# Kernel optimization log

Measured on AMD Instinct MI355X. Metric: run time of the kernel, lower is better.

The kernel has to match this reference:

```python
import jax, jax.numpy as jnp
import numpy as np

LEVELS = [(100, 128), (50, 64), (25, 32), (13, 16), (7, 8)]
B, C, S = 16, 80, 17064  # batch, class_num, sum(h*w)
GAMMA, ALPHA = 2.0, 0.25


def setup_inputs() -> dict:
    key = jax.random.key(0)
    ks = iter(jax.random.split(key, 40))
    inp = {}
    for i, (h, w) in enumerate(LEVELS):
        inp[f"cls_p{i}"] = jax.random.normal(next(ks), (B, C, h, w), dtype=jnp.float32)
        inp[f"cnt_p{i}"] = jax.random.normal(next(ks), (B, 1, h, w), dtype=jnp.float32)
        inp[f"reg_p{i}"] = jax.random.uniform(next(ks), (B, 4, h, w), dtype=jnp.float32) * 8.0 + 0.1
    keep = jax.random.uniform(next(ks), (B, S, 1)) > 0.7
    cnt_val = jax.random.uniform(next(ks), (B, S, 1), dtype=jnp.float32)
    inp["cnt_targets"] = jnp.where(keep, cnt_val, -1.0)
    inp["reg_targets"] = jax.random.uniform(next(ks), (B, S, 4), dtype=jnp.float32) * 8.0 + 0.1
    inp["cls_targets"] = jax.random.randint(next(ks), (B, S, 1), 0, 81, dtype=jnp.int64)
    return inp


def _flatten_levels(preds, c):
    # each pred [B,c,h,w] -> [B,h*w,c]; concat over levels -> [B,S,c]
    return jnp.concatenate(
        [p.transpose(0, 2, 3, 1).reshape(p.shape[0], -1, c) for p in preds], axis=1)


def _fcos_loss(cls_ps, cnt_ps, reg_ps, cls_t, cnt_t, reg_t):
    mask = (cnt_t > -1.0)[..., 0]                       # [B,S] bool positive mask
    num_pos = jnp.clip(jnp.sum(mask, axis=1), 1).astype(jnp.float32)  # [B]

    # ---- focal cls loss (over ALL locations, as in the original) ----
    cls = _flatten_levels(cls_ps, C)                    # [B,S,C]
    onehot = (jnp.arange(1, C + 1)[None, None, :] == cls_t).astype(jnp.float32)
    p = jax.nn.sigmoid(cls)
    p_t = onehot * p + (1.0 - onehot) * (1.0 - p)
    alpha_f = onehot * ALPHA + (1.0 - onehot) * (1.0 - ALPHA)
    focal = -alpha_f * (1.0 - p_t) ** GAMMA * jnp.log(p_t)
    cls_loss = jnp.mean(jnp.sum(focal, axis=(1, 2)) / num_pos)

    # ---- centerness BCE-with-logits, masked sum ----
    cnt = _flatten_levels(cnt_ps, 1)[..., 0]            # [B,S]
    t = cnt_t[..., 0]
    bce = jnp.maximum(cnt, 0.0) - cnt * t + jnp.log1p(jnp.exp(-jnp.abs(cnt)))
    cnt_loss = jnp.mean(jnp.sum(bce * mask, axis=1) / num_pos)

    # ---- GIoU reg loss, masked sum ----
    reg = _flatten_levels(reg_ps, 4)                    # [B,S,4] ltrb offsets
    lt_min = jnp.minimum(reg[..., :2], reg_t[..., :2])
    rb_min = jnp.minimum(reg[..., 2:], reg_t[..., 2:])
    wh_min = jnp.clip(rb_min + lt_min, 0.0)
    overlap = wh_min[..., 0] * wh_min[..., 1]
    area1 = (reg[..., 2] + reg[..., 0]) * (reg[..., 3] + reg[..., 1])
    area2 = (reg_t[..., 2] + reg_t[..., 0]) * (reg_t[..., 3] + reg_t[..., 1])
    union = area1 + area2 - overlap
    iou = overlap / union
    lt_max = jnp.maximum(reg[..., :2], reg_t[..., :2])
    rb_max = jnp.maximum(reg[..., 2:], reg_t[..., 2:])
    wh_max = jnp.clip(rb_max + lt_max, 0.0)
    g_area = wh_max[..., 0] * wh_max[..., 1]
    giou = iou - (g_area - union) / jnp.clip(g_area, 1e-10)
    reg_loss = jnp.mean(jnp.sum((1.0 - giou) * mask, axis=1) / num_pos)

    total = cls_loss + cnt_loss + reg_loss  # add_centerness=True
    return (cls_loss, cnt_loss, reg_loss, total)


def reference(cls_p0, cls_p1, cls_p2, cls_p3, cls_p4,
              cnt_p0, cnt_p1, cnt_p2, cnt_p3, cnt_p4,
              reg_p0, reg_p1, reg_p2, reg_p3, reg_p4,
              cnt_targets, reg_targets, cls_targets):
    return _fcos_loss([cls_p0, cls_p1, cls_p2, cls_p3, cls_p4],
                      [cnt_p0, cnt_p1, cnt_p2, cnt_p3, cnt_p4],
                      [reg_p0, reg_p1, reg_p2, reg_p3, reg_p4],
                      cls_targets, cnt_targets, reg_targets)
```

## Files before the change

### kernel.cpp

```cpp
#include <hip/hip_runtime.h>

#define S_TOTAL 17064
#define NB 16
#define NC 80
#define QPB 4266
#define NXQ 17
#define NCCH 20
#define NCH (NCCH + 1)
#define TOTAL_BLOCKS (NXQ * NCH * NB)
#define P1 TOTAL_BLOCKS
#define P2 (2 * TOTAL_BLOCKS)

typedef float vfloat4 __attribute__((ext_vector_type(4)));

struct Ptrs {
    const float* cls[5];
    const float* cnt[5];
    const float* reg[5];
    const float* cnt_t;
    const float* reg_t;
    const int*   cls_t;
    float*       ws;
    float*       out;
};

__device__ __forceinline__ float focal_term(float x, bool o) {
    const float xs = o ? x : -x;
    const float af = o ? 0.25f : 0.75f;
    const float em = __expf(-xs);
    const float pt = 1.0f / (1.0f + em);
    const float q  = em * pt;
    return af * q * q * __logf(1.0f + em);
}

__device__ __forceinline__ float giou_term(float pl, float pt_, float pr, float pb,
                                           float tl, float tt, float tr, float tb) {
    const float overlap = fmaxf(fminf(pr, tr) + fminf(pl, tl), 0.0f) *
                          fmaxf(fminf(pb, tb) + fminf(pt_, tt), 0.0f);
    const float area1 = (pr + pl) * (pb + pt_);
    const float area2 = (tr + tl) * (tb + tt);
    const float uni = area1 + area2 - overlap;
    const float iou = overlap / uni;
    const float ga = fmaxf(fmaxf(pr, tr) + fmaxf(pl, tl), 0.0f) *
                     fmaxf(fmaxf(pb, tb) + fmaxf(pt_, tt), 0.0f);
    const float giou = iou - (ga - uni) / fmaxf(ga, 1e-10f);
    return 1.0f - giou;
}

__device__ __forceinline__ float bce_term(float x, float t) {
    return fmaxf(x, 0.0f) - x * t + __logf(1.0f + __expf(-fabsf(x)));
}

__global__ __launch_bounds__(256) void fcos_main(Ptrs p) {
    const int xq = blockIdx.x;
    const int ch = blockIdx.y;
    const int b  = blockIdx.z;
    const int fq = xq * 256 + (int)threadIdx.x;

    int lvl, qb, hw, off;
    if (fq < 3200)      { lvl = 0; qb = 0;    hw = 12800; off = 0;     }
    else if (fq < 4000) { lvl = 1; qb = 3200; hw = 3200;  off = 12800; }
    else if (fq < 4200) { lvl = 2; qb = 4000; hw = 800;   off = 16000; }
    else if (fq < 4252) { lvl = 3; qb = 4200; hw = 208;   off = 16800; }
    else                { lvl = 4; qb = 4252; hw = 56;    off = 17008; }
    const bool active = (fq < QPB);

    float r0 = 0.f, r1 = 0.f, r2 = 0.f;

    if (active) {
        const int s0  = (fq - qb) << 2;
        const int gs0 = b * S_TOTAL + off + s0;

        if (ch < NCCH) {
            const int c0 = ch * 4;
            const int4 tq = *(const int4*)(p.cls_t + gs0);
            const float* cp = p.cls[lvl] + (size_t)((b * NC + c0) * hw + s0);

            vfloat4 buf[4];
            #pragma unroll
            for (int j = 0; j < 4; ++j)
                buf[j] = *(const vfloat4*)(cp + (size_t)(j * hw));

            float a0 = 0.f, a1 = 0.f, a2 = 0.f, a3 = 0.f;
            #pragma unroll
            for (int j = 0; j < 4; ++j) {
                const int c1 = c0 + j + 1;
                a0 += focal_term(buf[j].x, tq.x == c1);
                a1 += focal_term(buf[j].y, tq.y == c1);
                a2 += focal_term(buf[j].z, tq.z == c1);
                a3 += focal_term(buf[j].w, tq.w == c1);
            }
            r0 = (a0 + a1) + (a2 + a3);
        } else {
            const float4 tC  = *(const float4*)(p.cnt_t + gs0);
            const float4 xc  = *(const float4*)(p.cnt[lvl] + (size_t)(b * hw + s0));
            const float m0 = (tC.x > -1.0f) ? 1.0f : 0.0f;
            const float m1 = (tC.y > -1.0f) ? 1.0f : 0.0f;
            const float m2 = (tC.z > -1.0f) ? 1.0f : 0.0f;
            const float m3 = (tC.w > -1.0f) ? 1.0f : 0.0f;
            r2 = m0 + m1 + m2 + m3;
            r0 = bce_term(xc.x, tC.x) * m0 + bce_term(xc.y, tC.y) * m1 +
                 bce_term(xc.z, tC.z) * m2 + bce_term(xc.w, tC.w) * m3;

            const float* rp  = p.reg[lvl] + (size_t)(b * 4 * hw + s0);
            const float4 pl  = *(const float4*)(rp);
            const float4 pt_ = *(const float4*)(rp + (size_t)hw);
            const float4 pr  = *(const float4*)(rp + (size_t)(2 * hw));
            const float4 pb  = *(const float4*)(rp + (size_t)(3 * hw));
            const float4 t0  = *(const float4*)(p.reg_t + (size_t)(gs0 + 0) * 4);
            const float4 t1  = *(const float4*)(p.reg_t + (size_t)(gs0 + 1) * 4);
            const float4 t2  = *(const float4*)(p.reg_t + (size_t)(gs0 + 2) * 4);
            const float4 t3  = *(const float4*)(p.reg_t + (size_t)(gs0 + 3) * 4);

            r1 = giou_term(pl.x, pt_.x, pr.x, pb.x, t0.x, t0.y, t0.z, t0.w) * m0 +
                 giou_term(pl.y, pt_.y, pr.y, pb.y, t1.x, t1.y, t1.z, t1.w) * m1 +
                 giou_term(pl.z, pt_.z, pr.z, pb.z, t2.x, t2.y, t2.z, t2.w) * m2 +
                 giou_term(pl.w, pt_.w, pr.w, pb.w, t3.x, t3.y, t3.z, t3.w) * m3;
        }
    }

    #pragma unroll
    for (int d = 32; d; d >>= 1) {
        r0 += __shfl_down(r0, d);
        r1 += __shfl_down(r1, d);
        r2 += __shfl_down(r2, d);
    }

    __shared__ float red[3][4];
    const int wave = threadIdx.x >> 6;
    const int lane = threadIdx.x & 63;
    if (lane == 0) {
        red[0][wave] = r0;
        red[1][wave] = r1;
        red[2][wave] = r2;
    }
    __syncthreads();
    if (threadIdx.x == 0) {
        const int bid = xq + NXQ * (ch + NCH * b);
        p.ws[bid]      = red[0][0] + red[0][1] + red[0][2] + red[0][3];
        p.ws[P1 + bid] = red[1][0] + red[1][1] + red[1][2] + red[1][3];
        p.ws[P2 + bid] = red[2][0] + red[2][1] + red[2][2] + red[2][3];
    }
}

__global__ __launch_bounds__(512) void fcos_finalize(const float* __restrict__ ws,
                                                     float* __restrict__ out) {
    __shared__ float sA[NB * NCH];
    __shared__ float sB[NB * NCH];
    __shared__ float sC[NB * NCH];
    __shared__ float lb[3][NB];
    const int t = (int)threadIdx.x;

    if (t < NB * NCH) {
        const int b = t / NCH, ch = t - b * NCH;
        const int base = NXQ * (ch + NCH * b);
        float q0 = 0.f, q1 = 0.f, q2 = 0.f;
        #pragma unroll
        for (int xq = 0; xq < NXQ; ++xq) {
            q0 += ws[base + xq];
            q1 += ws[P1 + base + xq];
            q2 += ws[P2 + base + xq];
        }
        sA[t] = q0; sB[t] = q1; sC[t] = q2;
    }
    __syncthreads();

    if (t < NB) {
        const int rowbase = t * NCH;
        float cls = 0.f, reg = 0.f, pos = 0.f;
        #pragma unroll
        for (int ch = 0; ch < NCCH; ++ch) cls += sA[rowbase + ch];
        const float cnt = sA[rowbase + NCCH];
        #pragma unroll
        for (int ch = 0; ch < NCH; ++ch) { reg += sB[rowbase + ch]; pos += sC[rowbase + ch]; }
        const float np = fmaxf(pos, 1.0f);
        lb[0][t] = cls / np;
        lb[1][t] = cnt / np;
        lb[2][t] = reg / np;
    }
    __syncthreads();

    if (t == 0) {
        float l0 = 0.f, l1 = 0.f, l2 = 0.f;
        #pragma unroll
        for (int b = 0; b < NB; ++b) {
            l0 += lb[0][b]; l1 += lb[1][b]; l2 += lb[2][b];
        }
        l0 *= (1.0f / NB); l1 *= (1.0f / NB); l2 *= (1.0f / NB);
        out[0] = l0;
        out[1] = l1;
        out[2] = l2;
        out[3] = l0 + l1 + l2;
    }
}

extern "C" void kernel_launch(void* const* d_in, const int* in_sizes, int n_in,
                              void* d_out, int out_size, void* d_ws, size_t ws_size,
                              hipStream_t stream) {
    Ptrs p;
    for (int i = 0; i < 5; ++i) {
        p.cls[i] = (const float*)d_in[3 * i + 0];
        p.cnt[i] = (const float*)d_in[3 * i + 1];
        p.reg[i] = (const float*)d_in[3 * i + 2];
    }
    p.cnt_t = (const float*)d_in[15];
    p.reg_t = (const float*)d_in[16];
    p.cls_t = (const int*)  d_in[17];
    p.ws    = (float*)d_ws;
    p.out   = (float*)d_out;

    dim3 grid(NXQ, NCH, NB);
    fcos_main<<<grid, 256, 0, stream>>>(p);
    fcos_finalize<<<dim3(1), 512, 0, stream>>>((const float*)d_ws, (float*)d_out);
}
```

Measured before the change: 152.7 us.

## Regroup work into 7 channel chunks per block, folding cnt/reg into last chunk

Each block now processes 12 classification channels (8 in the last chunk) and the last chunk also computes the centerness and GIoU terms, in place of 20 four-channel class blocks plus a separate cnt/reg block. This cuts the grid from 21 to 7 chunks per position tile and reloads class targets less often, with more work per thread. The finalize kernel changes to a strided 256-thread reduction over four partial arrays. The risks are fewer blocks to hide latency with, and imbalance because the last chunk carries the extra cnt/reg work.

After: 149.1 us. 1.02x faster.

```diff
diff --git a/kernel.cpp b/kernel.cpp
--- a/kernel.cpp
+++ b/kernel.cpp
@@ -5,11 +5,9 @@
 #define NC 80
 #define QPB 4266
 #define NXQ 17
-#define NCCH 20
-#define NCH (NCCH + 1)
-#define TOTAL_BLOCKS (NXQ * NCH * NB)
-#define P1 TOTAL_BLOCKS
-#define P2 (2 * TOTAL_BLOCKS)
+#define NJ 7
+#define TOTAL_BLOCKS (NB * NJ * NXQ)
+#define PL TOTAL_BLOCKS
 
 typedef float vfloat4 __attribute__((ext_vector_type(4)));
 
@@ -52,10 +50,12 @@
 }
 
 __global__ __launch_bounds__(256) void fcos_main(Ptrs p) {
-    const int xq = blockIdx.x;
-    const int ch = blockIdx.y;
-    const int b  = blockIdx.z;
-    const int fq = xq * 256 + (int)threadIdx.x;
+    const int bid = (int)blockIdx.x;
+    const int b   = bid / (NJ * NXQ);
+    const int r   = bid - b * (NJ * NXQ);
+    const int j   = r / NXQ;
+    const int xq  = r - j * NXQ;
+    const int fq  = xq * 256 + (int)threadIdx.x;
 
     int lvl, qb, hw, off;
     if (fq < 3200)      { lvl = 0; qb = 0;    hw = 12800; off = 0;     }
@@ -65,42 +65,39 @@
     else                { lvl = 4; qb = 4252; hw = 56;    off = 17008; }
     const bool active = (fq < QPB);
 
-    float r0 = 0.f, r1 = 0.f, r2 = 0.f;
+    float acls = 0.f, acnt = 0.f, areg = 0.f, apos = 0.f;
 
     if (active) {
         const int s0  = (fq - qb) << 2;
         const int gs0 = b * S_TOTAL + off + s0;
-
-        if (ch < NCCH) {
-            const int c0 = ch * 4;
-            const int4 tq = *(const int4*)(p.cls_t + gs0);
-            const float* cp = p.cls[lvl] + (size_t)((b * NC + c0) * hw + s0);
-
-            vfloat4 buf[4];
-            #pragma unroll
-            for (int j = 0; j < 4; ++j)
-                buf[j] = *(const vfloat4*)(cp + (size_t)(j * hw));
-
-            float a0 = 0.f, a1 = 0.f, a2 = 0.f, a3 = 0.f;
-            #pragma unroll
-            for (int j = 0; j < 4; ++j) {
-                const int c1 = c0 + j + 1;
-                a0 += focal_term(buf[j].x, tq.x == c1);
-                a1 += focal_term(buf[j].y, tq.y == c1);
-                a2 += focal_term(buf[j].z, tq.z == c1);
-                a3 += focal_term(buf[j].w, tq.w == c1);
-            }
-            r0 = (a0 + a1) + (a2 + a3);
-        } else {
+        const int4 tq = *(const int4*)(p.cls_t + gs0);
+
+        const int cbase = j * 12;
+        const int ncls  = (j < 6) ? 12 : 8;
+        const float* cp = p.cls[lvl] + (size_t)((b * NC + cbase) * hw + s0);
+
+        float a0 = 0.f, a1 = 0.f, a2 = 0.f, a3 = 0.f;
+        #pragma unroll 4
+        for (int c = 0; c < ncls; ++c) {
+            const vfloat4 v = *(const vfloat4*)(cp + (size_t)(c * hw));
+            const int c1 = cbase + c + 1;
+            a0 += focal_term(v.x, tq.x == c1);
+            a1 += focal_term(v.y, tq.y == c1);
+            a2 += focal_term(v.z, tq.z == c1);
+            a3 += focal_term(v.w, tq.w == c1);
+        }
+        acls = (a0 + a1) + (a2 + a3);
+
+        if (j == 6) {
             const float4 tC  = *(const float4*)(p.cnt_t + gs0);
             const float4 xc  = *(const float4*)(p.cnt[lvl] + (size_t)(b * hw + s0));
             const float m0 = (tC.x > -1.0f) ? 1.0f : 0.0f;
             const float m1 = (tC.y > -1.0f) ? 1.0f : 0.0f;
             const float m2 = (tC.z > -1.0f) ? 1.0f : 0.0f;
             const float m3 = (tC.w > -1.0f) ? 1.0f : 0.0f;
-            r2 = m0 + m1 + m2 + m3;
-            r0 = bce_term(xc.x, tC.x) * m0 + bce_term(xc.y, tC.y) * m1 +
-                 bce_term(xc.z, tC.z) * m2 + bce_term(xc.w, tC.w) * m3;
+            apos = m0 + m1 + m2 + m3;
+            acnt = bce_term(xc.x, tC.x) * m0 + bce_term(xc.y, tC.y) * m1 +
+                   bce_term(xc.z, tC.z) * m2 + bce_term(xc.w, tC.w) * m3;
 
             const float* rp  = p.reg[lvl] + (size_t)(b * 4 * hw + s0);
             const float4 pl  = *(const float4*)(rp);
@@ -112,67 +109,67 @@
             const float4 t2  = *(const float4*)(p.reg_t + (size_t)(gs0 + 2) * 4);
             const float4 t3  = *(const float4*)(p.reg_t + (size_t)(gs0 + 3) * 4);
 
-            r1 = giou_term(pl.x, pt_.x, pr.x, pb.x, t0.x, t0.y, t0.z, t0.w) * m0 +
-                 giou_term(pl.y, pt_.y, pr.y, pb.y, t1.x, t1.y, t1.z, t1.w) * m1 +
-                 giou_term(pl.z, pt_.z, pr.z, pb.z, t2.x, t2.y, t2.z, t2.w) * m2 +
-                 giou_term(pl.w, pt_.w, pr.w, pb.w, t3.x, t3.y, t3.z, t3.w) * m3;
+            areg = giou_term(pl.x, pt_.x, pr.x, pb.x, t0.x, t0.y, t0.z, t0.w) * m0 +
+                   giou_term(pl.y, pt_.y, pr.y, pb.y, t1.x, t1.y, t1.z, t1.w) * m1 +
+                   giou_term(pl.z, pt_.z, pr.z, pb.z, t2.x, t2.y, t2.z, t2.w) * m2 +
+                   giou_term(pl.w, pt_.w, pr.w, pb.w, t3.x, t3.y, t3.z, t3.w) * m3;
         }
     }
 
     #pragma unroll
     for (int d = 32; d; d >>= 1) {
-        r0 += __shfl_down(r0, d);
-        r1 += __shfl_down(r1, d);
-        r2 += __shfl_down(r2, d);
-    }
-
-    __shared__ float red[3][4];
+        acls += __shfl_down(acls, d);
+        acnt += __shfl_down(acnt, d);
+        areg += __shfl_down(areg, d);
+        apos += __shfl_down(apos, d);
+    }
+
+    __shared__ float red[4][4];
     const int wave = threadIdx.x >> 6;
     const int lane = threadIdx.x & 63;
     if (lane == 0) {
-        red[0][wave] = r0;
-        red[1][wave] = r1;
-        red[2][wave] = r2;
+        red[0][wave] = acls;
+        red[1][wave] = acnt;
+        red[2][wave] = areg;
+        red[3][wave] = apos;
     }
     __syncthreads();
     if (threadIdx.x == 0) {
-        const int bid = xq + NXQ * (ch + NCH * b);
-        p.ws[bid]      = red[0][0] + red[0][1] + red[0][2] + red[0][3];
-        p.ws[P1 + bid] = red[1][0] + red[1][1] + red[1][2] + red[1][3];
-        p.ws[P2 + bid] = red[2][0] + red[2][1] + red[2][2] + red[2][3];
-    }
-}
-
-__global__ __launch_bounds__(512) void fcos_finalize(const float* __restrict__ ws,
+        p.ws[bid]          = red[0][0] + red[0][1] + red[0][2] + red[0][3];
+        p.ws[PL + bid]     = red[1][0] + red[1][1] + red[1][2] + red[1][3];
+        p.ws[2 * PL + bid] = red[2][0] + red[2][1] + red[2][2] + red[2][3];
+        p.ws[3 * PL + bid] = red[3][0] + red[3][1] + red[3][2] + red[3][3];
+    }
+}
+
+__global__ __launch_bounds__(256) void fcos_finalize(const float* __restrict__ ws,
                                                      float* __restrict__ out) {
-    __shared__ float sA[NB * NCH];
-    __shared__ float sB[NB * NCH];
-    __shared__ float sC[NB * NCH];
+    __shared__ float s[4][256];
     __shared__ float lb[3][NB];
     const int t = (int)threadIdx.x;
-
-    if (t < NB * NCH) {
-        const int b = t / NCH, ch = t - b * NCH;
-        const int base = NXQ * (ch + NCH * b);
-        float q0 = 0.f, q1 = 0.f, q2 = 0.f;
+    const int b = t >> 4;
+    const int k = t & 15;
+
+    float q0 = 0.f, q1 = 0.f, q2 = 0.f, q3 = 0.f;
+    for (int i = k; i < NJ * NXQ; i += 16) {
+        const int slot = b * (NJ * NXQ) + i;
+        q0 += ws[slot];
+        q1 += ws[PL + slot];
+        q2 += ws[2 * PL + slot];
+        q3 += ws[3 * PL + slot];
+    }
+    s[0][t] = q0; s[1][t] = q1; s[2][t] = q2; s[3][t] = q3;
+    __syncthreads();
+
+    if (t < NB) {
+        float cls = 0.f, cnt = 0.f, reg = 0.f, pos = 0.f;
         #pragma unroll
-        for (int xq = 0; xq < NXQ; ++xq) {
-            q0 += ws[base + xq];
-            q1 += ws[P1 + base + xq];
-            q2 += ws[P2 + base + xq];
-        }
-        sA[t] = q0; sB[t] = q1; sC[t] = q2;
-    }
-    __syncthreads();
-
-    if (t < NB) {
-        const int rowbase = t * NCH;
-        float cls = 0.f, reg = 0.f, pos = 0.f;
-        #pragma unroll
-        for (int ch = 0; ch < NCCH; ++ch) cls += sA[rowbase + ch];
-        const float cnt = sA[rowbase + NCCH];
-        #pragma unroll
-        for (int ch = 0; ch < NCH; ++ch) { reg += sB[rowbase + ch]; pos += sC[rowbase + ch]; }
+        for (int kk = 0; kk < 16; ++kk) {
+            cls += s[0][t * 16 + kk];
+            cnt += s[1][t * 16 + kk];
+            reg += s[2][t * 16 + kk];
+            pos += s[3][t * 16 + kk];
+        }
         const float np = fmaxf(pos, 1.0f);
         lb[0][t] = cls / np;
         lb[1][t] = cnt / np;
@@ -183,8 +180,8 @@
     if (t == 0) {
         float l0 = 0.f, l1 = 0.f, l2 = 0.f;
         #pragma unroll
-        for (int b = 0; b < NB; ++b) {
-            l0 += lb[0][b]; l1 += lb[1][b]; l2 += lb[2][b];
+        for (int bb = 0; bb < NB; ++bb) {
+            l0 += lb[0][bb]; l1 += lb[1][bb]; l2 += lb[2][bb];
         }
         l0 *= (1.0f / NB); l1 *= (1.0f / NB); l2 *= (1.0f / NB);
         out[0] = l0;
@@ -209,7 +206,6 @@
     p.ws    = (float*)d_ws;
     p.out   = (float*)d_out;
 
-    dim3 grid(NXQ, NCH, NB);
-    fcos_main<<<grid, 256, 0, stream>>>(p);
-    fcos_finalize<<<dim3(1), 512, 0, stream>>>((const float*)d_ws, (float*)d_out);
-}
+    fcos_main<<<dim3(TOTAL_BLOCKS), 256, 0, stream>>>(p);
+    fcos_finalize<<<dim3(1), 256, 0, stream>>>((const float*)d_ws, (float*)d_out);
+}
```
